# Performance work log

Measured on AMD Instinct MI355X. Metric: run time of the kernel, lower is better.

The kernel has to match this reference:

```python
import jax, jax.numpy as jnp
import numpy as np

N_NODES = 8192
N_EDGES = 524288
D_IN = 256
D_OUT = 256


def setup_inputs() -> dict:
    key = jax.random.key(0)
    ks = jax.random.split(key, 8)
    h = jax.random.normal(ks[0], (N_NODES, D_IN), dtype=jnp.float32)
    # Xavier-uniform-like scale for weights
    s = (6.0 / (D_IN + D_OUT)) ** 0.5
    W = jax.random.uniform(ks[1], (D_IN, D_OUT), jnp.float32, -s, s)
    Wq = jax.random.uniform(ks[2], (D_IN, D_OUT), jnp.float32, -s, s)
    bq = jnp.zeros((D_OUT,), jnp.float32)
    Wk = jax.random.uniform(ks[3], (D_IN, D_OUT), jnp.float32, -s, s)
    bk = jnp.zeros((D_OUT,), jnp.float32)
    senders = jax.random.randint(ks[4], (N_EDGES,), 0, N_NODES, dtype=jnp.int64 if jax.config.jax_enable_x64 else jnp.int32)
    receivers = jax.random.randint(ks[5], (N_EDGES,), 0, N_NODES, dtype=jnp.int64 if jax.config.jax_enable_x64 else jnp.int32)
    return {"h": h, "W": W, "Wq": Wq, "bq": bq, "Wk": Wk, "bk": bk,
            "senders": senders, "receivers": receivers}


def reference(h, W, Wq, bq, Wk, bk, senders, receivers):
    # Projected node features: (N, D_OUT)
    h_proj = jnp.dot(h, W)
    # Dense attention logits a = q @ k^T: (N, N), as in the original module
    q = jnp.dot(h, Wq) + bq
    k = jnp.dot(h, Wk) + bk
    a = jnp.dot(q, k.T)
    # Gather per-edge messages and attention weights, weight, scatter-add
    messages = h_proj[senders] * a[senders, receivers][:, None]  # (E, D_OUT)
    aggregated = jax.ops.segment_sum(messages, receivers, num_segments=h.shape[0])
    return jax.nn.relu(aggregated)
```

## Files before the change

kernel.cpp:

```cpp
#include <hip/hip_runtime.h>
#include <stdint.h>

typedef unsigned short u16;
typedef unsigned int u32;
typedef short v8s __attribute__((ext_vector_type(8)));
typedef float v4f __attribute__((ext_vector_type(4)));

#define N_NODES 8192
#define N_EDGES 524288
#define DFEAT 256
#define PADC 160
#define CNTS 16

static __device__ __forceinline__ float bflo(u32 u) { return __uint_as_float(u << 16); }
static __device__ __forceinline__ float bfhi(u32 u) { return __uint_as_float(u & 0xffff0000u); }
static __device__ __forceinline__ u16 f2bf(float f) {
    u32 u = __float_as_uint(f);
    return (u16)((u + 0x7fffu + ((u >> 16) & 1u)) >> 16);
}

__global__ void prep_small(const float* __restrict__ w0, const float* __restrict__ w1,
                           const float* __restrict__ w2, u16* __restrict__ wt,
                           int* __restrict__ cnt) {
    int b = blockIdx.x;
    if (b < 48) {
        __shared__ u16 t[64][65];
        int region = b >> 4, tile = b & 15;
        int k0 = (tile >> 2) * 64, n0 = (tile & 3) * 64;
        const float* w = (region == 0) ? w0 : ((region == 1) ? w1 : w2);
        int tx = threadIdx.x & 63, ty = threadIdx.x >> 6;
#pragma unroll
        for (int it = 0; it < 16; it++) {
            int row = it * 4 + ty;
            t[row][tx] = f2bf(w[(k0 + row) * 256 + n0 + tx]);
        }
        __syncthreads();
        u16* o = wt + region * 65536;
#pragma unroll
        for (int it = 0; it < 16; it++) {
            int row = it * 4 + ty;
            o[(n0 + row) * 256 + k0 + tx] = t[tx][row];
        }
    } else {
        int i = ((b - 48) * 256 + threadIdx.x) * 4;
        *(int4*)(cnt + i) = make_int4(0, 0, 0, 0);
    }
}

__global__ __launch_bounds__(256) void main_mid(
    const float* __restrict__ h, const u16* __restrict__ wt,
    const float* __restrict__ bq, const float* __restrict__ bk,
    const int* __restrict__ recv, const int* __restrict__ send,
    u16* __restrict__ hproj, u16* __restrict__ qbuf, u16* __restrict__ kbuf,
    int* __restrict__ cnt, u16* __restrict__ es) {
    int b = blockIdx.x;
    if (b < 2048) {
        int e = b * 256 + threadIdx.x;
        int r = recv[e];
        int s = send[e];
        int pos = atomicAdd(&cnt[r * CNTS], 1);
        if (pos < PADC) es[r * PADC + pos] = (u16)s;
    } else {
        int g = b - 2048;
        int wave = threadIdx.x >> 6, lane = threadIdx.x & 63;
        int lm = lane & 15, lq = lane >> 4;
        int bx = g & 127, by = g >> 7;
        int m0 = bx * 64 + wave * 16;
        int region = by >> 2, n0b = (by & 3) * 64;
        const u16* wtr = wt + region * 65536;

        v4f acc[4];
#pragma unroll
        for (int nt = 0; nt < 4; nt++) acc[nt] = (v4f){0.f, 0.f, 0.f, 0.f};

        const float* arow = h + (m0 + lm) * 256 + lq * 8;
#pragma unroll
        for (int k0 = 0; k0 < 256; k0 += 32) {
            float4 f0 = *(const float4*)(arow + k0);
            float4 f1 = *(const float4*)(arow + k0 + 4);
            v8s a;
            a[0] = (short)f2bf(f0.x); a[1] = (short)f2bf(f0.y);
            a[2] = (short)f2bf(f0.z); a[3] = (short)f2bf(f0.w);
            a[4] = (short)f2bf(f1.x); a[5] = (short)f2bf(f1.y);
            a[6] = (short)f2bf(f1.z); a[7] = (short)f2bf(f1.w);
#pragma unroll
            for (int nt = 0; nt < 4; nt++) {
                v8s bb = *(const v8s*)(wtr + (n0b + nt * 16 + lm) * 256 + k0 + lq * 8);
                acc[nt] = __builtin_amdgcn_mfma_f32_16x16x32_bf16(a, bb, acc[nt], 0, 0, 0);
            }
        }
        u16* outp = (region == 0) ? hproj : ((region == 1) ? qbuf : kbuf);
        const float* bias = (region == 1) ? bq : ((region == 2) ? bk : nullptr);
#pragma unroll
        for (int nt = 0; nt < 4; nt++) {
            int nn = n0b + nt * 16 + lm;
            float bv = bias ? bias[nn] : 0.f;
#pragma unroll
            for (int i = 0; i < 4; i++) {
                int m = m0 + lq * 4 + i;
                outp[m * 256 + nn] = f2bf(acc[nt][i] + bv);
            }
        }
    }
}


#define DOT8(Q) (kr0 * bflo((Q).x) + kr1 * bfhi((Q).x)                        \
               + kr2 * bflo((Q).y) + kr3 * bfhi((Q).y)                        \
               + kr4 * bflo((Q).z) + kr5 * bfhi((Q).z)                        \
               + kr6 * bflo((Q).w) + kr7 * bfhi((Q).w))

#define AXPY(P, H) do {                                                       \
    a0 += (P) * bflo((H).x); a1 += (P) * bfhi((H).x);                         \
    a2 += (P) * bflo((H).y); a3 += (P) * bfhi((H).y);                         \
    a4 += (P) * bflo((H).z); a5 += (P) * bfhi((H).z);                         \
    a6 += (P) * bflo((H).w); a7 += (P) * bfhi((H).w);                         \
} while (0)

#define DOT_AGG1(SIDX) do {                                                   \
    int off_ = (int)(SIDX) * 256 + cb;                                        \
    uint4 qv_ = *(const uint4*)(qbuf + off_);                                 \
    uint4 hv_ = *(const uint4*)(hpb + off_);                                  \
    float p_ = DOT8(qv_);                                                     \
    p_ += __shfl_xor(p_, 1, 32);  p_ += __shfl_xor(p_, 2, 32);                \
    p_ += __shfl_xor(p_, 4, 32);  p_ += __shfl_xor(p_, 8, 32);                \
    p_ += __shfl_xor(p_, 16, 32);                                             \
    AXPY(p_, hv_);                                                            \
} while (0)

#define LOAD4(P, SP) do {                                                     \
    int s0_ = (int)((SP).x & 0xffffu), s1_ = (int)((SP).x >> 16);             \
    int s2_ = (int)((SP).y & 0xffffu), s3_ = (int)((SP).y >> 16);             \
    q##P##0 = *(const uint4*)(qbuf + s0_ * 256 + cb);                         \
    h##P##0 = *(const uint4*)(hpb  + s0_ * 256 + cb);                         \
    q##P##1 = *(const uint4*)(qbuf + s1_ * 256 + cb);                         \
    h##P##1 = *(const uint4*)(hpb  + s1_ * 256 + cb);                         \
    q##P##2 = *(const uint4*)(qbuf + s2_ * 256 + cb);                         \
    h##P##2 = *(const uint4*)(hpb  + s2_ * 256 + cb);                         \
    q##P##3 = *(const uint4*)(qbuf + s3_ * 256 + cb);                         \
    h##P##3 = *(const uint4*)(hpb  + s3_ * 256 + cb);                         \
} while (0)

#define COMP4(P) do {                                                         \
    float p0_ = DOT8(q##P##0), p1_ = DOT8(q##P##1);                           \
    float p2_ = DOT8(q##P##2), p3_ = DOT8(q##P##3);                           \
    p0_ += __shfl_xor(p0_, 1, 32);  p1_ += __shfl_xor(p1_, 1, 32);            \
    p2_ += __shfl_xor(p2_, 1, 32);  p3_ += __shfl_xor(p3_, 1, 32);            \
    p0_ += __shfl_xor(p0_, 2, 32);  p1_ += __shfl_xor(p1_, 2, 32);            \
    p2_ += __shfl_xor(p2_, 2, 32);  p3_ += __shfl_xor(p3_, 2, 32);            \
    p0_ += __shfl_xor(p0_, 4, 32);  p1_ += __shfl_xor(p1_, 4, 32);            \
    p2_ += __shfl_xor(p2_, 4, 32);  p3_ += __shfl_xor(p3_, 4, 32);            \
    p0_ += __shfl_xor(p0_, 8, 32);  p1_ += __shfl_xor(p1_, 8, 32);            \
    p2_ += __shfl_xor(p2_, 8, 32);  p3_ += __shfl_xor(p3_, 8, 32);            \
    p0_ += __shfl_xor(p0_, 16, 32); p1_ += __shfl_xor(p1_, 16, 32);           \
    p2_ += __shfl_xor(p2_, 16, 32); p3_ += __shfl_xor(p3_, 16, 32);           \
    AXPY(p0_, h##P##0); AXPY(p1_, h##P##1);                                   \
    AXPY(p2_, h##P##2); AXPY(p3_, h##P##3);                                   \
} while (0)

#define STAGE(CUR, NXT, TC) do {                                              \
    if ((TC) + 1 < NT) {                                                      \
        LOAD4(NXT, spn);                                                      \
        if ((TC) + 2 < NT)                                                    \
            spn = *(const uint2*)(es + base + ((TC) + 2) * 8 + half * 4);     \
    }                                                                         \
    COMP4(CUR);                                                               \
} while (0)

__global__ __launch_bounds__(256, 4) void edge_fused(
    const u16* __restrict__ qbuf, const u16* __restrict__ kbuf,
    const u16* __restrict__ hpb, const int* __restrict__ cnt,
    const u16* __restrict__ es, float* __restrict__ out) {
    int wave = threadIdx.x >> 6, lane = threadIdx.x & 63;
    int r = blockIdx.x * 4 + wave;
    int lh = lane & 31, half = lane >> 5;
    int cb = lh * 8;
    int n = min(cnt[r * CNTS], PADC);
    int base = r * PADC;

    uint4 kv = *(const uint4*)(kbuf + r * 256 + cb);
    float kr0 = bflo(kv.x), kr1 = bfhi(kv.x), kr2 = bflo(kv.y), kr3 = bfhi(kv.y),
          kr4 = bflo(kv.z), kr5 = bfhi(kv.z), kr6 = bflo(kv.w), kr7 = bfhi(kv.w);

    float a0 = 0.f, a1 = 0.f, a2 = 0.f, a3 = 0.f,
          a4 = 0.f, a5 = 0.f, a6 = 0.f, a7 = 0.f;

    int NT = n >> 3;
    int m  = n & 7;

    if (NT > 0) {
        uint4 qc0, qc1, qc2, qc3, hc0, hc1, hc2, hc3;
        uint4 qn0, qn1, qn2, qn3, hn0, hn1, hn2, hn3;
        uint2 spc = *(const uint2*)(es + base + half * 4);
        LOAD4(c, spc);
        uint2 spn = spc;
        if (NT > 1) spn = *(const uint2*)(es + base + 8 + half * 4);
        for (int t = 0; t < NT; t += 2) {
            STAGE(c, n, t);
            if (t + 1 < NT) STAGE(n, c, t + 1);
        }
    }
    if (m > 0) {
        uint2 spT = *(const uint2*)(es + base + NT * 8 + half * 4);
        int mrem = m - half * 4;
        if (mrem > 0) DOT_AGG1(spT.x & 0xffffu);
        if (mrem > 1) DOT_AGG1(spT.x >> 16);
        if (mrem > 2) DOT_AGG1(spT.y & 0xffffu);
        if (mrem > 3) DOT_AGG1(spT.y >> 16);
    }

    a0 += __shfl_xor(a0, 32, 64); a1 += __shfl_xor(a1, 32, 64);
    a2 += __shfl_xor(a2, 32, 64); a3 += __shfl_xor(a3, 32, 64);
    a4 += __shfl_xor(a4, 32, 64); a5 += __shfl_xor(a5, 32, 64);
    a6 += __shfl_xor(a6, 32, 64); a7 += __shfl_xor(a7, 32, 64);

    if (half == 0) {
        float4 o0, o1;
        o0.x = fmaxf(a0, 0.f); o0.y = fmaxf(a1, 0.f);
        o0.z = fmaxf(a2, 0.f); o0.w = fmaxf(a3, 0.f);
        o1.x = fmaxf(a4, 0.f); o1.y = fmaxf(a5, 0.f);
        o1.z = fmaxf(a6, 0.f); o1.w = fmaxf(a7, 0.f);
        float* op = out + r * 256 + cb;
        *(float4*)op = o0;
        *(float4*)(op + 4) = o1;
    }
}

extern "C" void kernel_launch(void* const* d_in, const int* in_sizes, int n_in,
                              void* d_out, int out_size, void* d_ws, size_t ws_size,
                              hipStream_t stream) {
    const float* h  = (const float*)d_in[0];
    const float* W  = (const float*)d_in[1];
    const float* Wq = (const float*)d_in[2];
    const float* bq = (const float*)d_in[3];
    const float* Wk = (const float*)d_in[4];
    const float* bk = (const float*)d_in[5];
    const int* senders   = (const int*)d_in[6];
    const int* receivers = (const int*)d_in[7];
    float* out = (float*)d_out;

    char* ws = (char*)d_ws;
    u16* wt    = (u16*)ws;
    u16* hproj = (u16*)(ws + 393216);
    u16* qbuf  = hproj + N_NODES * DFEAT;
    u16* kbuf  = qbuf + N_NODES * DFEAT;
    int* cnt   = (int*)(kbuf + N_NODES * DFEAT);
    u16* es    = (u16*)(cnt + N_NODES * CNTS);

    prep_small<<<176, 256, 0, stream>>>(W, Wq, Wk, wt, cnt);
    main_mid<<<3584, 256, 0, stream>>>(h, wt, bq, bk, receivers, senders,
                                       hproj, qbuf, kbuf, cnt, es);
    edge_fused<<<N_NODES / 4, 256, 0, stream>>>(qbuf, kbuf, hproj, cnt, es, out);
}
```

Measured before the change: 181.0 us.

## Replace global-atomic edge bucketing with LDS histogram, scan, and placement passes

Edge bucketing by receiver used to run as one global atomicAdd per edge on padded counters, sharing a launch with the projection GEMM. It now runs as three kernels: per-block LDS histograms over edge chunks, a column-wise exclusive scan across blocks, and a placement pass that uses LDS atomics on the scanned offsets. The GEMM becomes its own launch, and zeroing the counters is no longer needed. The aim is to remove contended global atomics, but the change adds three serial launches, and the histogram and placement passes use only 64 blocks each, which may leave most of the GPU idle and serialize work that used to overlap with the GEMM.

```diff
diff --git a/kernel.cpp b/kernel.cpp
--- a/kernel.cpp
+++ b/kernel.cpp
@@ -10,7 +10,8 @@
 #define N_EDGES 524288
 #define DFEAT 256
 #define PADC 160
-#define CNTS 16
+#define NHB 64
+#define EPB (N_EDGES / NHB)
 
 static __device__ __forceinline__ float bflo(u32 u) { return __uint_as_float(u << 16); }
 static __device__ __forceinline__ float bfhi(u32 u) { return __uint_as_float(u & 0xffff0000u); }
@@ -20,86 +21,125 @@
 }
 
 __global__ void prep_small(const float* __restrict__ w0, const float* __restrict__ w1,
-                           const float* __restrict__ w2, u16* __restrict__ wt,
-                           int* __restrict__ cnt) {
+                           const float* __restrict__ w2, u16* __restrict__ wt) {
+    __shared__ u16 t[64][65];
     int b = blockIdx.x;
-    if (b < 48) {
-        __shared__ u16 t[64][65];
-        int region = b >> 4, tile = b & 15;
-        int k0 = (tile >> 2) * 64, n0 = (tile & 3) * 64;
-        const float* w = (region == 0) ? w0 : ((region == 1) ? w1 : w2);
-        int tx = threadIdx.x & 63, ty = threadIdx.x >> 6;
-#pragma unroll
-        for (int it = 0; it < 16; it++) {
-            int row = it * 4 + ty;
-            t[row][tx] = f2bf(w[(k0 + row) * 256 + n0 + tx]);
-        }
-        __syncthreads();
-        u16* o = wt + region * 65536;
-#pragma unroll
-        for (int it = 0; it < 16; it++) {
-            int row = it * 4 + ty;
-            o[(n0 + row) * 256 + k0 + tx] = t[tx][row];
-        }
-    } else {
-        int i = ((b - 48) * 256 + threadIdx.x) * 4;
-        *(int4*)(cnt + i) = make_int4(0, 0, 0, 0);
-    }
-}
-
-__global__ __launch_bounds__(256) void main_mid(
+    int region = b >> 4, tile = b & 15;
+    int k0 = (tile >> 2) * 64, n0 = (tile & 3) * 64;
+    const float* w = (region == 0) ? w0 : ((region == 1) ? w1 : w2);
+    int tx = threadIdx.x & 63, ty = threadIdx.x >> 6;
+#pragma unroll
+    for (int it = 0; it < 16; it++) {
+        int row = it * 4 + ty;
+        t[row][tx] = f2bf(w[(k0 + row) * 256 + n0 + tx]);
+    }
+    __syncthreads();
+    u16* o = wt + region * 65536;
+#pragma unroll
+    for (int it = 0; it < 16; it++) {
+        int row = it * 4 + ty;
+        o[(n0 + row) * 256 + k0 + tx] = t[tx][row];
+    }
+}
+
+__global__ __launch_bounds__(256) void hist_k(const int* __restrict__ recv,
+                                              int* __restrict__ ghist) {
+    __shared__ int hist[N_NODES];
+    for (int i = threadIdx.x; i < N_NODES; i += 256) hist[i] = 0;
+    __syncthreads();
+    int e0 = blockIdx.x * EPB;
+    for (int i = threadIdx.x; i < EPB; i += 256)
+        atomicAdd(&hist[recv[e0 + i]], 1);
+    __syncthreads();
+    int* gh = ghist + blockIdx.x * N_NODES;
+    for (int i = threadIdx.x; i < N_NODES; i += 256) gh[i] = hist[i];
+}
+
+__global__ __launch_bounds__(256) void scan_k(int* __restrict__ ghist,
+                                              int* __restrict__ cnt) {
+    int r = blockIdx.x * 256 + threadIdx.x;
+    int run = 0;
+#pragma unroll
+    for (int b0 = 0; b0 < NHB; b0 += 8) {
+        int t0 = ghist[(b0 + 0) * N_NODES + r];
+        int t1 = ghist[(b0 + 1) * N_NODES + r];
+        int t2 = ghist[(b0 + 2) * N_NODES + r];
+        int t3 = ghist[(b0 + 3) * N_NODES + r];
+        int t4 = ghist[(b0 + 4) * N_NODES + r];
+        int t5 = ghist[(b0 + 5) * N_NODES + r];
+        int t6 = ghist[(b0 + 6) * N_NODES + r];
+        int t7 = ghist[(b0 + 7) * N_NODES + r];
+        ghist[(b0 + 0) * N_NODES + r] = run; run += t0;
+        ghist[(b0 + 1) * N_NODES + r] = run; run += t1;
+        ghist[(b0 + 2) * N_NODES + r] = run; run += t2;
+        ghist[(b0 + 3) * N_NODES + r] = run; run += t3;
+        ghist[(b0 + 4) * N_NODES + r] = run; run += t4;
+        ghist[(b0 + 5) * N_NODES + r] = run; run += t5;
+        ghist[(b0 + 6) * N_NODES + r] = run; run += t6;
+        ghist[(b0 + 7) * N_NODES + r] = run; run += t7;
+    }
+    cnt[r] = run;
+}
+
+__global__ __launch_bounds__(256) void place_k(const int* __restrict__ recv,
+                                               const int* __restrict__ send,
+                                               const int* __restrict__ ghist,
+                                               u16* __restrict__ es) {
+    __shared__ int off[N_NODES];
+    const int* gh = ghist + blockIdx.x * N_NODES;
+    for (int i = threadIdx.x; i < N_NODES; i += 256) off[i] = gh[i];
+    __syncthreads();
+    int e0 = blockIdx.x * EPB;
+    for (int i = threadIdx.x; i < EPB; i += 256) {
+        int r = recv[e0 + i];
+        int s = send[e0 + i];
+        int pos = atomicAdd(&off[r], 1);
+        if (pos < PADC) es[r * PADC + pos] = (u16)s;
+    }
+}
+
+__global__ __launch_bounds__(256) void gemm_k(
     const float* __restrict__ h, const u16* __restrict__ wt,
     const float* __restrict__ bq, const float* __restrict__ bk,
-    const int* __restrict__ recv, const int* __restrict__ send,
-    u16* __restrict__ hproj, u16* __restrict__ qbuf, u16* __restrict__ kbuf,
-    int* __restrict__ cnt, u16* __restrict__ es) {
-    int b = blockIdx.x;
-    if (b < 2048) {
-        int e = b * 256 + threadIdx.x;
-        int r = recv[e];
-        int s = send[e];
-        int pos = atomicAdd(&cnt[r * CNTS], 1);
-        if (pos < PADC) es[r * PADC + pos] = (u16)s;
-    } else {
-        int g = b - 2048;
-        int wave = threadIdx.x >> 6, lane = threadIdx.x & 63;
-        int lm = lane & 15, lq = lane >> 4;
-        int bx = g & 127, by = g >> 7;
-        int m0 = bx * 64 + wave * 16;
-        int region = by >> 2, n0b = (by & 3) * 64;
-        const u16* wtr = wt + region * 65536;
-
-        v4f acc[4];
-#pragma unroll
-        for (int nt = 0; nt < 4; nt++) acc[nt] = (v4f){0.f, 0.f, 0.f, 0.f};
-
-        const float* arow = h + (m0 + lm) * 256 + lq * 8;
-#pragma unroll
-        for (int k0 = 0; k0 < 256; k0 += 32) {
-            float4 f0 = *(const float4*)(arow + k0);
-            float4 f1 = *(const float4*)(arow + k0 + 4);
-            v8s a;
-            a[0] = (short)f2bf(f0.x); a[1] = (short)f2bf(f0.y);
-            a[2] = (short)f2bf(f0.z); a[3] = (short)f2bf(f0.w);
-            a[4] = (short)f2bf(f1.x); a[5] = (short)f2bf(f1.y);
-            a[6] = (short)f2bf(f1.z); a[7] = (short)f2bf(f1.w);
-#pragma unroll
-            for (int nt = 0; nt < 4; nt++) {
-                v8s bb = *(const v8s*)(wtr + (n0b + nt * 16 + lm) * 256 + k0 + lq * 8);
-                acc[nt] = __builtin_amdgcn_mfma_f32_16x16x32_bf16(a, bb, acc[nt], 0, 0, 0);
-            }
+    u16* __restrict__ hproj, u16* __restrict__ qbuf, u16* __restrict__ kbuf) {
+    int g = blockIdx.x;
+    int wave = threadIdx.x >> 6, lane = threadIdx.x & 63;
+    int lm = lane & 15, lq = lane >> 4;
+    int bx = g & 127, by = g >> 7;
+    int m0 = bx * 64 + wave * 16;
+    int region = by >> 2, n0b = (by & 3) * 64;
+    const u16* wtr = wt + region * 65536;
+
+    v4f acc[4];
+#pragma unroll
+    for (int nt = 0; nt < 4; nt++) acc[nt] = (v4f){0.f, 0.f, 0.f, 0.f};
+
+    const float* arow = h + (m0 + lm) * 256 + lq * 8;
+#pragma unroll
+    for (int k0 = 0; k0 < 256; k0 += 32) {
+        float4 f0 = *(const float4*)(arow + k0);
+        float4 f1 = *(const float4*)(arow + k0 + 4);
+        v8s a;
+        a[0] = (short)f2bf(f0.x); a[1] = (short)f2bf(f0.y);
+        a[2] = (short)f2bf(f0.z); a[3] = (short)f2bf(f0.w);
+        a[4] = (short)f2bf(f1.x); a[5] = (short)f2bf(f1.y);
+        a[6] = (short)f2bf(f1.z); a[7] = (short)f2bf(f1.w);
+#pragma unroll
+        for (int nt = 0; nt < 4; nt++) {
+            v8s bb = *(const v8s*)(wtr + (n0b + nt * 16 + lm) * 256 + k0 + lq * 8);
+            acc[nt] = __builtin_amdgcn_mfma_f32_16x16x32_bf16(a, bb, acc[nt], 0, 0, 0);
         }
-        u16* outp = (region == 0) ? hproj : ((region == 1) ? qbuf : kbuf);
-        const float* bias = (region == 1) ? bq : ((region == 2) ? bk : nullptr);
-#pragma unroll
-        for (int nt = 0; nt < 4; nt++) {
-            int nn = n0b + nt * 16 + lm;
-            float bv = bias ? bias[nn] : 0.f;
-#pragma unroll
-            for (int i = 0; i < 4; i++) {
-                int m = m0 + lq * 4 + i;
-                outp[m * 256 + nn] = f2bf(acc[nt][i] + bv);
-            }
+    }
+    u16* outp = (region == 0) ? hproj : ((region == 1) ? qbuf : kbuf);
+    const float* bias = (region == 1) ? bq : ((region == 2) ? bk : nullptr);
+#pragma unroll
+    for (int nt = 0; nt < 4; nt++) {
+        int nn = n0b + nt * 16 + lm;
+        float bv = bias ? bias[nn] : 0.f;
+#pragma unroll
+        for (int i = 0; i < 4; i++) {
+            int m = m0 + lq * 4 + i;
+            outp[m * 256 + nn] = f2bf(acc[nt][i] + bv);
         }
     }
 }
@@ -175,7 +215,7 @@
     int r = blockIdx.x * 4 + wave;
     int lh = lane & 31, half = lane >> 5;
     int cb = lh * 8;
-    int n = min(cnt[r * CNTS], PADC);
+    int n = min(cnt[r], PADC);
     int base = r * PADC;
 
     uint4 kv = *(const uint4*)(kbuf + r * 256 + cb);
@@ -245,10 +285,13 @@
     u16* qbuf  = hproj + N_NODES * DFEAT;
     u16* kbuf  = qbuf + N_NODES * DFEAT;
     int* cnt   = (int*)(kbuf + N_NODES * DFEAT);
-    u16* es    = (u16*)(cnt + N_NODES * CNTS);
-
-    prep_small<<<176, 256, 0, stream>>>(W, Wq, Wk, wt, cnt);
-    main_mid<<<3584, 256, 0, stream>>>(h, wt, bq, bk, receivers, senders,
-                                       hproj, qbuf, kbuf, cnt, es);
+    u16* es    = (u16*)(cnt + N_NODES);
+    int* ghist = (int*)(es + N_NODES * PADC);
+
+    prep_small<<<48, 256, 0, stream>>>(W, Wq, Wk, wt);
+    hist_k<<<NHB, 256, 0, stream>>>(receivers, ghist);
+    scan_k<<<N_NODES / 256, 256, 0, stream>>>(ghist, cnt);
+    place_k<<<NHB, 256, 0, stream>>>(receivers, senders, ghist, es);
+    gemm_k<<<1536, 256, 0, stream>>>(h, wt, bq, bk, hproj, qbuf, kbuf);
     edge_fused<<<N_NODES / 4, 256, 0, stream>>>(qbuf, kbuf, hproj, cnt, es, out);
 }
```

New measurement: 191.4 us. +5.8%, slower.

## Replace global atomic edge binning with two-pass LDS bucket sort

Applied to the files above, without the earlier changes.

Edge binning by receiver used to do one global atomic per edge on a padded counter array. It now does a two-pass bucketing. First, 128 blocks each histogram and locally sort their slice of edges into 128 coarse buckets in LDS and reserve global ranges with one atomic per bucket. A new partB kernel then scatters each bucket into per-receiver lists in LDS and writes them out coalesced. This cuts global atomic contention and scattered writes, at the cost of an extra kernel launch and an intermediate bucket buffer with a fixed capacity that could overflow.

```diff
diff --git a/kernel.cpp b/kernel.cpp
--- a/kernel.cpp
+++ b/kernel.cpp
@@ -10,7 +10,10 @@
 #define N_EDGES 524288
 #define DFEAT 256
 #define PADC 160
-#define CNTS 16
+#define NBKT 128
+#define NPA  128
+#define EPA  (N_EDGES / NPA)
+#define EBCAP 4608
 
 static __device__ __forceinline__ float bflo(u32 u) { return __uint_as_float(u << 16); }
 static __device__ __forceinline__ float bfhi(u32 u) { return __uint_as_float(u & 0xffff0000u); }
@@ -21,7 +24,7 @@
 
 __global__ void prep_small(const float* __restrict__ w0, const float* __restrict__ w1,
                            const float* __restrict__ w2, u16* __restrict__ wt,
-                           int* __restrict__ cnt) {
+                           int* __restrict__ bcnt) {
     int b = blockIdx.x;
     if (b < 48) {
         __shared__ u16 t[64][65];
@@ -42,27 +45,69 @@
             o[(n0 + row) * 256 + k0 + tx] = t[tx][row];
         }
     } else {
-        int i = ((b - 48) * 256 + threadIdx.x) * 4;
-        *(int4*)(cnt + i) = make_int4(0, 0, 0, 0);
-    }
-}
-
-__global__ __launch_bounds__(256) void main_mid(
+        if (threadIdx.x < NBKT) bcnt[threadIdx.x] = 0;
+    }
+}
+
+__global__ __launch_bounds__(256) void partA_gemm(
     const float* __restrict__ h, const u16* __restrict__ wt,
     const float* __restrict__ bq, const float* __restrict__ bk,
     const int* __restrict__ recv, const int* __restrict__ send,
     u16* __restrict__ hproj, u16* __restrict__ qbuf, u16* __restrict__ kbuf,
-    int* __restrict__ cnt, u16* __restrict__ es) {
+    u32* __restrict__ ebuck, int* __restrict__ bcnt) {
     int b = blockIdx.x;
-    if (b < 2048) {
-        int e = b * 256 + threadIdx.x;
-        int r = recv[e];
-        int s = send[e];
-        int pos = atomicAdd(&cnt[r * CNTS], 1);
-        if (pos < PADC) es[r * PADC + pos] = (u16)s;
+    int tid = threadIdx.x;
+    if (b < NPA) {
+        __shared__ int hist[NBKT];
+        __shared__ int lstart[NBKT + 1];
+        __shared__ int cursor[NBKT];
+        __shared__ int gpos[NBKT];
+        __shared__ u32 sorted[EPA];
+        int e0 = b * EPA;
+        int r_[16], s_[16];
+#pragma unroll
+        for (int i = 0; i < 16; i++) {
+            int e = e0 + i * 256 + tid;
+            r_[i] = recv[e];
+            s_[i] = send[e];
+        }
+        if (tid < NBKT) hist[tid] = 0;
+        __syncthreads();
+#pragma unroll
+        for (int i = 0; i < 16; i++) atomicAdd(&hist[r_[i] >> 6], 1);
+        __syncthreads();
+        if (tid == 0) {
+            int run = 0;
+            for (int k = 0; k < NBKT; k++) { lstart[k] = run; run += hist[k]; }
+            lstart[NBKT] = run;
+        }
+        __syncthreads();
+        if (tid < NBKT) {
+            cursor[tid] = lstart[tid];
+            gpos[tid] = atomicAdd(&bcnt[tid], hist[tid]);
+        }
+        __syncthreads();
+#pragma unroll
+        for (int i = 0; i < 16; i++) {
+            int key = r_[i] >> 6;
+            int pos = atomicAdd(&cursor[key], 1);
+            sorted[pos] = ((u32)r_[i] << 13) | (u32)s_[i];
+        }
+        __syncthreads();
+        for (int i = tid; i < EPA; i += 256) {
+            int lo = 0, hi = NBKT - 1;
+#pragma unroll
+            for (int it = 0; it < 7; it++) {
+                int mid = (lo + hi + 1) >> 1;
+                if (lstart[mid] <= i) lo = mid; else hi = mid - 1;
+            }
+            int k = lo;
+            int dst = gpos[k] + (i - lstart[k]);
+            if (dst < EBCAP) ebuck[k * EBCAP + dst] = sorted[i];
+        }
     } else {
-        int g = b - 2048;
-        int wave = threadIdx.x >> 6, lane = threadIdx.x & 63;
+        int g = b - NPA;
+        int wave = tid >> 6, lane = tid & 63;
         int lm = lane & 15, lq = lane >> 4;
         int bx = g & 127, by = g >> 7;
         int m0 = bx * 64 + wave * 16;
@@ -102,6 +147,32 @@
             }
         }
     }
+}
+
+__global__ __launch_bounds__(256) void partB(const u32* __restrict__ ebuck,
+                                             const int* __restrict__ bcnt,
+                                             u16* __restrict__ es,
+                                             int* __restrict__ cnt) {
+    __shared__ int off[64];
+    __shared__ uint4 imgv[64 * PADC * 2 / 16];
+    u16* image = (u16*)imgv;
+    int k = blockIdx.x;
+    int tid = threadIdx.x;
+    if (tid < 64) off[tid] = 0;
+    __syncthreads();
+    int size = min(bcnt[k], EBCAP);
+    const u32* eb = ebuck + k * EBCAP;
+    for (int i = tid; i < size; i += 256) {
+        u32 v = eb[i];
+        int rl = (int)(v >> 13) & 63;
+        int s  = (int)(v & 8191u);
+        int pos = atomicAdd(&off[rl], 1);
+        if (pos < PADC) image[rl * PADC + pos] = (u16)s;
+    }
+    __syncthreads();
+    uint4* dst = (uint4*)(es + k * 64 * PADC);
+    for (int i = tid; i < 64 * PADC * 2 / 16; i += 256) dst[i] = imgv[i];
+    if (tid < 64) cnt[k * 64 + tid] = off[tid];
 }
 
 
@@ -175,7 +246,7 @@
     int r = blockIdx.x * 4 + wave;
     int lh = lane & 31, half = lane >> 5;
     int cb = lh * 8;
-    int n = min(cnt[r * CNTS], PADC);
+    int n = min(cnt[r], PADC);
     int base = r * PADC;
 
     uint4 kv = *(const uint4*)(kbuf + r * 256 + cb);
@@ -245,10 +316,13 @@
     u16* qbuf  = hproj + N_NODES * DFEAT;
     u16* kbuf  = qbuf + N_NODES * DFEAT;
     int* cnt   = (int*)(kbuf + N_NODES * DFEAT);
-    u16* es    = (u16*)(cnt + N_NODES * CNTS);
-
-    prep_small<<<176, 256, 0, stream>>>(W, Wq, Wk, wt, cnt);
-    main_mid<<<3584, 256, 0, stream>>>(h, wt, bq, bk, receivers, senders,
-                                       hproj, qbuf, kbuf, cnt, es);
+    u16* es    = (u16*)(cnt + N_NODES);
+    u32* ebuck = (u32*)(es + N_NODES * PADC);
+    int* bcnt  = (int*)(ebuck + NBKT * EBCAP);
+
+    prep_small<<<49, 256, 0, stream>>>(W, Wq, Wk, wt, bcnt);
+    partA_gemm<<<NPA + 1536, 256, 0, stream>>>(h, wt, bq, bk, receivers, senders,
+                                               hproj, qbuf, kbuf, ebuck, bcnt);
+    partB<<<NBKT, 256, 0, stream>>>(ebuck, bcnt, es, cnt);
     edge_fused<<<N_NODES / 4, 256, 0, stream>>>(qbuf, kbuf, hproj, cnt, es, out);
 }
```

New measurement: 164.0 us. -9.4%, faster.
